# Optimization experiments

Hardware: AMD Instinct MI355X
Metric: run time of the kernel (lower is better)

## Reference

```python
import jax, jax.numpy as jnp
import numpy as np

B, TQ, TK, H = 8, 64, 8192, 256


def setup_inputs() -> dict:
    key = jax.random.key(0)
    k1, k2, k3, k4 = jax.random.split(key, 4)
    query = jax.random.normal(k1, (B, TQ, H), dtype=jnp.float32)
    keys = jax.random.normal(k2, (B, TK, H), dtype=jnp.float32)
    # nn.Linear(H, H): weight [H, H], bias [H]; scale like torch default-ish
    Wa_w = jax.random.normal(k3, (H, H), dtype=jnp.float32) * (1.0 / np.sqrt(H))
    Wa_b = jax.random.normal(k4, (H,), dtype=jnp.float32) * 0.01
    return {"query": query, "keys": keys, "Wa_w": Wa_w, "Wa_b": Wa_b}


def reference(query, keys, Wa_w, Wa_b):
    # keys_transformed = keys @ Wa_w.T + Wa_b  (torch Linear semantics)
    keys_t = jnp.einsum('bkh,oh->bko', keys, Wa_w) + Wa_b  # [B,TK,H]
    scores = jnp.einsum('bqh,bkh->bqk', query, keys_t)       # [B,TQ,TK]
    weights = jax.nn.softmax(scores, axis=-1)
    context = jnp.einsum('bqk,bkh->bqh', weights, keys)      # [B,TQ,H]
    return (context, weights)
```

## Files before the change

kernel.cpp:

```cpp
#include <hip/hip_runtime.h>

#define B 8
#define TQ 64
#define TK 8192
#define H 256

#define SPADB 72

#define KSPLIT 32
#define KPB (TK / KSPLIT)
#define CRS 72

typedef __attribute__((ext_vector_type(8))) short bf16x8;
typedef __attribute__((ext_vector_type(4))) float f32x4;
typedef __attribute__((ext_vector_type(4))) unsigned short u16x4;
typedef __attribute__((ext_vector_type(2))) unsigned int u32x2;

static __device__ inline unsigned short f2bf_rne(float x) {
    unsigned int u = __float_as_uint(x);
    unsigned int r = (u + 0x7fffu + ((u >> 16) & 1u)) >> 16;
    return (unsigned short)r;
}

__global__ __launch_bounds__(256) void qtransform_kernel(
    const float* __restrict__ query, const float* __restrict__ Wa_w,
    const float* __restrict__ Wa_b, unsigned short* __restrict__ qthi,
    unsigned short* __restrict__ qtlo, float* __restrict__ qb)
{
    __shared__ float q_s[H];
    __shared__ float red[4];
    const int r = blockIdx.x;
    const int t = threadIdx.x;
    q_s[t] = query[r * H + t];
    __syncthreads();

    float a0 = 0.f, a1 = 0.f, a2 = 0.f, a3 = 0.f;
    for (int o = 0; o < H; o += 4) {
        a0 += q_s[o + 0] * Wa_w[(o + 0) * H + t];
        a1 += q_s[o + 1] * Wa_w[(o + 1) * H + t];
        a2 += q_s[o + 2] * Wa_w[(o + 2) * H + t];
        a3 += q_s[o + 3] * Wa_w[(o + 3) * H + t];
    }
    const float s = (a0 + a1) + (a2 + a3);
    const unsigned int u = __float_as_uint(s);
    const float hif = __uint_as_float(u & 0xFFFF0000u);
    const float lof = s - hif;
    qthi[r * H + t] = (unsigned short)(u >> 16);
    qtlo[r * H + t] = (unsigned short)(__float_as_uint(lof) >> 16);

    float p = q_s[t] * Wa_b[t];
    for (int off = 32; off > 0; off >>= 1) p += __shfl_down(p, off, 64);
    if ((t & 63) == 0) red[t >> 6] = p;
    __syncthreads();
    if (t == 0) qb[r] = (red[0] + red[1]) + (red[2] + red[3]);
}

__global__ __launch_bounds__(256) void scores_kernel(
    const unsigned short* __restrict__ qthi, const unsigned short* __restrict__ qtlo,
    const float* __restrict__ qb, const float* __restrict__ keys,
    unsigned short* __restrict__ khi_ws, float* __restrict__ wout)
{
    __shared__ unsigned short a_hi[TQ][SPADB], a_lo[TQ][SPADB];
    __shared__ unsigned short b_hi[64][SPADB], b_lo[64][SPADB];
    const int t    = threadIdx.x;
    const int kt   = blockIdx.x;
    const int b    = blockIdx.y;
    const int k0g  = kt * 64;
    const int w    = t >> 6;
    const int lane = t & 63;
    const int lrow = lane & 15;
    const int lgrp = lane >> 4;

    f32x4 acc[4];
    #pragma unroll
    for (int nt = 0; nt < 4; ++nt) acc[nt] = (f32x4){0.f, 0.f, 0.f, 0.f};

    for (int hc = 0; hc < H; hc += 64) {
        __syncthreads();
        #pragma unroll
        for (int i = 0; i < 4; ++i) {
            int idx = t + 256 * i;
            int row = idx >> 4, hf = idx & 15;
            *(u16x4*)&a_hi[row][hf * 4] =
                *(const u16x4*)&qthi[(b * TQ + row) * H + hc + hf * 4];
            *(u16x4*)&a_lo[row][hf * 4] =
                *(const u16x4*)&qtlo[(b * TQ + row) * H + hc + hf * 4];
        }
        #pragma unroll
        for (int i = 0; i < 4; ++i) {
            int idx = t + 256 * i;
            int row = idx >> 4, hf = idx & 15;
            float4 vb = *(const float4*)&keys[(size_t)(b * TK + k0g + row) * H + hc + hf * 4];
            unsigned int u0 = __float_as_uint(vb.x), u1 = __float_as_uint(vb.y);
            unsigned int u2 = __float_as_uint(vb.z), u3 = __float_as_uint(vb.w);
            unsigned int h01 = (u0 >> 16) | (u1 & 0xFFFF0000u);
            unsigned int h23 = (u2 >> 16) | (u3 & 0xFFFF0000u);
            float l0 = vb.x - __uint_as_float(u0 & 0xFFFF0000u);
            float l1 = vb.y - __uint_as_float(u1 & 0xFFFF0000u);
            float l2 = vb.z - __uint_as_float(u2 & 0xFFFF0000u);
            float l3 = vb.w - __uint_as_float(u3 & 0xFFFF0000u);
            unsigned int l01 = (__float_as_uint(l0) >> 16) | (__float_as_uint(l1) & 0xFFFF0000u);
            unsigned int l23 = (__float_as_uint(l2) >> 16) | (__float_as_uint(l3) & 0xFFFF0000u);
            *(u32x2*)&b_hi[row][hf * 4] = (u32x2){h01, h23};
            *(u32x2*)&b_lo[row][hf * 4] = (u32x2){l01, l23};
            *(u32x2*)&khi_ws[((size_t)b * TK + k0g + row) * H + hc + hf * 4] = (u32x2){h01, h23};
        }
        __syncthreads();
        #pragma unroll
        for (int hs = 0; hs < 64; hs += 32) {
            bf16x8 ah = *(const bf16x8*)&a_hi[16 * w + lrow][hs + lgrp * 8];
            bf16x8 al = *(const bf16x8*)&a_lo[16 * w + lrow][hs + lgrp * 8];
            #pragma unroll
            for (int nt = 0; nt < 4; ++nt) {
                bf16x8 bh = *(const bf16x8*)&b_hi[16 * nt + lrow][hs + lgrp * 8];
                bf16x8 bl = *(const bf16x8*)&b_lo[16 * nt + lrow][hs + lgrp * 8];
                acc[nt] = __builtin_amdgcn_mfma_f32_16x16x32_bf16(ah, bh, acc[nt], 0, 0, 0);
                acc[nt] = __builtin_amdgcn_mfma_f32_16x16x32_bf16(ah, bl, acc[nt], 0, 0, 0);
                acc[nt] = __builtin_amdgcn_mfma_f32_16x16x32_bf16(al, bh, acc[nt], 0, 0, 0);
            }
        }
    }
    #pragma unroll
    for (int j = 0; j < 4; ++j) {
        const int qrow = 16 * w + lgrp * 4 + j;
        const float bias = qb[b * TQ + qrow];
        float* dst = &wout[(size_t)(b * TQ + qrow) * TK + k0g + lrow];
        #pragma unroll
        for (int nt = 0; nt < 4; ++nt) dst[16 * nt] = acc[nt][j] + bias;
    }
}

__global__ __launch_bounds__(1024) void softmax_kernel(
    float* __restrict__ w, unsigned short* __restrict__ phi)
{
    const int r = blockIdx.x;
    const int t = threadIdx.x;
    float4* row4 = (float4*)(w + (size_t)r * TK);
    __shared__ float redm[16];
    __shared__ float reds[16];
    const int wid = t >> 6, lane = t & 63;

    float4 v0 = row4[t];
    float4 v1 = row4[t + 1024];
    float m = fmaxf(fmaxf(fmaxf(v0.x, v0.y), fmaxf(v0.z, v0.w)),
                    fmaxf(fmaxf(v1.x, v1.y), fmaxf(v1.z, v1.w)));
    for (int off = 32; off > 0; off >>= 1) m = fmaxf(m, __shfl_xor(m, off, 64));
    if (lane == 0) redm[wid] = m;
    __syncthreads();
    m = redm[0];
    #pragma unroll
    for (int i = 1; i < 16; ++i) m = fmaxf(m, redm[i]);

    v0.x = __expf(v0.x - m); v0.y = __expf(v0.y - m);
    v0.z = __expf(v0.z - m); v0.w = __expf(v0.w - m);
    v1.x = __expf(v1.x - m); v1.y = __expf(v1.y - m);
    v1.z = __expf(v1.z - m); v1.w = __expf(v1.w - m);
    float s = (v0.x + v0.y + v0.z + v0.w) + (v1.x + v1.y + v1.z + v1.w);
    for (int off = 32; off > 0; off >>= 1) s += __shfl_xor(s, off, 64);
    if (lane == 0) reds[wid] = s;
    __syncthreads();
    s = reds[0];
    #pragma unroll
    for (int i = 1; i < 16; ++i) s += reds[i];
    const float inv = 1.0f / s;

    v0.x *= inv; v0.y *= inv; v0.z *= inv; v0.w *= inv;
    v1.x *= inv; v1.y *= inv; v1.z *= inv; v1.w *= inv;
    row4[t] = v0;
    row4[t + 1024] = v1;

    unsigned short* prow = phi + (size_t)r * TK;
    u16x4 p0, p1;
    p0[0] = f2bf_rne(v0.x); p0[1] = f2bf_rne(v0.y);
    p0[2] = f2bf_rne(v0.z); p0[3] = f2bf_rne(v0.w);
    p1[0] = f2bf_rne(v1.x); p1[1] = f2bf_rne(v1.y);
    p1[2] = f2bf_rne(v1.z); p1[3] = f2bf_rne(v1.w);
    *(u16x4*)&prow[t * 4] = p0;
    *(u16x4*)&prow[4096 + t * 4] = p1;
}

__global__ __launch_bounds__(256) void context_main_kernel(
    const unsigned short* __restrict__ phi, const unsigned short* __restrict__ khi,
    float* __restrict__ part)
{
    __shared__ unsigned short kT[64 * CRS];
    const int t    = threadIdx.x;
    const int ks   = blockIdx.x;
    const int ht   = blockIdx.y;
    const int b    = blockIdx.z;
    const int w    = t >> 6;
    const int lane = t & 63;
    const int lrow = lane & 15;
    const int lgrp = lane >> 4;

    f32x4 acc[4];
    #pragma unroll
    for (int nt = 0; nt < 4; ++nt) acc[nt] = (f32x4){0.f, 0.f, 0.f, 0.f};

    const int kbase = ks * KPB;
    for (int c = 0; c < KPB; c += 64) {
        __syncthreads();
        #pragma unroll
        for (int i = 0; i < 4; ++i) {
            int idx = t + 256 * i;
            int k = idx >> 4, hq = idx & 15;
            u16x4 v = *(const u16x4*)&khi[((size_t)b * TK + kbase + c + k) * H + ht * 64 + hq * 4];
            #pragma unroll
            for (int c4 = 0; c4 < 4; ++c4) {
                int h = hq * 4 + c4;
                kT[h * CRS + (((k >> 3) ^ ((h >> 3) & 7)) << 3) + (k & 7)] = v[c4];
            }
        }
        __syncthreads();
        #pragma unroll
        for (int kc = 0; kc < 64; kc += 32) {
            bf16x8 af = *(const bf16x8*)&phi[((size_t)(b * TQ) + 16 * w + lrow) * TK
                                             + kbase + c + kc + lgrp * 8];
            #pragma unroll
            for (int nt = 0; nt < 4; ++nt) {
                int h = 16 * nt + lrow;
                bf16x8 bf = *(const bf16x8*)&kT[h * CRS
                              + ((((kc >> 3) + lgrp) ^ ((h >> 3) & 7)) << 3)];
                acc[nt] = __builtin_amdgcn_mfma_f32_16x16x32_bf16(af, bf, acc[nt], 0, 0, 0);
            }
        }
    }
    float* dst = part + (size_t)ks * (B * TQ * H);
    #pragma unroll
    for (int j = 0; j < 4; ++j) {
        const int qrow = 16 * w + lgrp * 4 + j;
        #pragma unroll
        for (int nt = 0; nt < 4; ++nt)
            dst[(size_t)(b * TQ + qrow) * H + ht * 64 + 16 * nt + lrow] = acc[nt][j];
    }
}

__global__ __launch_bounds__(256) void context_reduce_kernel(
    const float* __restrict__ part, float* __restrict__ ctx)
{
    const int idx = blockIdx.x * 256 + threadIdx.x;
    float4 s = make_float4(0.f, 0.f, 0.f, 0.f);
    #pragma unroll 8
    for (int ks = 0; ks < KSPLIT; ++ks) {
        float4 v = *(const float4*)&part[(size_t)ks * (B * TQ * H) + (size_t)idx * 4];
        s.x += v.x; s.y += v.y; s.z += v.z; s.w += v.w;
    }
    *(float4*)&ctx[(size_t)idx * 4] = s;
}

extern "C" void kernel_launch(void* const* d_in, const int* in_sizes, int n_in,
                              void* d_out, int out_size, void* d_ws, size_t ws_size,
                              hipStream_t stream) {
    const float* query = (const float*)d_in[0];
    const float* keys  = (const float*)d_in[1];
    const float* Wa_w  = (const float*)d_in[2];
    const float* Wa_b  = (const float*)d_in[3];

    float* ctx = (float*)d_out;
    float* wts = (float*)d_out + B * TQ * H;

    char* p = (char*)d_ws;
    float* part = (float*)p;            p += (size_t)KSPLIT * B * TQ * H * 4;
    unsigned short* khi = (unsigned short*)p;  p += (size_t)B * TK * H * 2;
    unsigned short* phi = (unsigned short*)p;  p += (size_t)B * TQ * TK * 2;
    unsigned short* qthi = (unsigned short*)p; p += (size_t)B * TQ * H * 2;
    unsigned short* qtlo = (unsigned short*)p; p += (size_t)B * TQ * H * 2;
    float* qb = (float*)p;

    qtransform_kernel<<<B * TQ, 256, 0, stream>>>(query, Wa_w, Wa_b, qthi, qtlo, qb);
    scores_kernel<<<dim3(TK / 64, B), 256, 0, stream>>>(qthi, qtlo, qb, keys, khi, wts);
    softmax_kernel<<<B * TQ, 1024, 0, stream>>>(wts, phi);
    context_main_kernel<<<dim3(KSPLIT, 4, B), 256, 0, stream>>>(phi, khi, part);
    context_reduce_kernel<<<(B * TQ * H / 4) / 256, 256, 0, stream>>>(part, ctx);
}
```

Before: 158.9 us.

## Store bf16 keys transposed, double-buffer scores staging, drop LDS in context GEMM

The scores kernel now writes the bf16 keys copy transposed ([B,H,TK]) so the context GEMM can load B-fragments directly from global memory, with no LDS transpose and no barriers. The scores kernel reads query fragments straight from global instead of staging them through LDS. It also double-buffers the key tiles with register prefetch of the next chunk, and uses an XOR-swizzled unpadded LDS layout. The transposed key writes are 2-byte scattered stores with stride TK, which may be poorly coalesced and could slow the scores kernel.

Result: slower. 187.5 us (+18.0%).

```diff
diff --git a/kernel.cpp b/kernel.cpp
--- a/kernel.cpp
+++ b/kernel.cpp
@@ -5,11 +5,8 @@
 #define TK 8192
 #define H 256
 
-#define SPADB 72
-
 #define KSPLIT 32
 #define KPB (TK / KSPLIT)
-#define CRS 72
 
 typedef __attribute__((ext_vector_type(8))) short bf16x8;
 typedef __attribute__((ext_vector_type(4))) float f32x4;
@@ -55,13 +52,59 @@
     if (t == 0) qb[r] = (red[0] + red[1]) + (red[2] + red[3]);
 }
 
-__global__ __launch_bounds__(256) void scores_kernel(
+
+#define STAGE1(v, row, buf, khb) {                                             \
+    unsigned int u0=__float_as_uint(v.x), u1=__float_as_uint(v.y);             \
+    unsigned int u2=__float_as_uint(v.z), u3=__float_as_uint(v.w);             \
+    unsigned int h01=(u0>>16)|(u1&0xFFFF0000u), h23=(u2>>16)|(u3&0xFFFF0000u); \
+    float l0=v.x-__uint_as_float(u0&0xFFFF0000u);                              \
+    float l1=v.y-__uint_as_float(u1&0xFFFF0000u);                              \
+    float l2=v.z-__uint_as_float(u2&0xFFFF0000u);                              \
+    float l3=v.w-__uint_as_float(u3&0xFFFF0000u);                              \
+    unsigned int q01=(__float_as_uint(l0)>>16)|(__float_as_uint(l1)&0xFFFF0000u); \
+    unsigned int q23=(__float_as_uint(l2)>>16)|(__float_as_uint(l3)&0xFFFF0000u); \
+    int bo=(row)*128 + (((hf>>1)^((row)&7))<<4) + ((hf&1)<<3);                 \
+    *(u32x2*)((char*)b_hi[buf]+bo) = (u32x2){h01,h23};                         \
+    *(u32x2*)((char*)b_lo[buf]+bo) = (u32x2){q01,q23};                         \
+    khb[(size_t)(hf*4+0)*TK + (row)] = (unsigned short)(u0>>16);               \
+    khb[(size_t)(hf*4+1)*TK + (row)] = (unsigned short)(u1>>16);               \
+    khb[(size_t)(hf*4+2)*TK + (row)] = (unsigned short)(u2>>16);               \
+    khb[(size_t)(hf*4+3)*TK + (row)] = (unsigned short)(u3>>16); }
+
+#define LOADCHUNK(d0,d1,d2,d3, hc)                                             \
+    d0 = *(const float4*)&kbase_g[(size_t)(sr +  0) * H + (hc) + hf * 4];      \
+    d1 = *(const float4*)&kbase_g[(size_t)(sr + 16) * H + (hc) + hf * 4];      \
+    d2 = *(const float4*)&kbase_g[(size_t)(sr + 32) * H + (hc) + hf * 4];      \
+    d3 = *(const float4*)&kbase_g[(size_t)(sr + 48) * H + (hc) + hf * 4];
+
+#define STAGECHUNK(v0,v1,v2,v3, buf, hc) {                                     \
+    unsigned short* khb = khiT + ((size_t)b * H + (hc)) * TK + k0g;            \
+    STAGE1(v0, sr +  0, buf, khb); STAGE1(v1, sr + 16, buf, khb);              \
+    STAGE1(v2, sr + 32, buf, khb); STAGE1(v3, sr + 48, buf, khb); }
+
+#define COMPUTE(buf, hc) {                                                     \
+    _Pragma("unroll")                                                          \
+    for (int hs = 0; hs < 64; hs += 32) {                                      \
+        bf16x8 ah = *(const bf16x8*)&ah_base[(hc) + hs + lgrp * 8];            \
+        bf16x8 al = *(const bf16x8*)&al_base[(hc) + hs + lgrp * 8];            \
+        _Pragma("unroll")                                                      \
+        for (int nt = 0; nt < 4; ++nt) {                                       \
+            int rr = 16 * nt + lrow;                                           \
+            int rb = rr * 128 + ((((hs >> 3) + lgrp) ^ (rr & 7)) << 4);        \
+            bf16x8 bh = *(const bf16x8*)((const char*)b_hi[buf] + rb);         \
+            bf16x8 bl = *(const bf16x8*)((const char*)b_lo[buf] + rb);         \
+            acc[nt] = __builtin_amdgcn_mfma_f32_16x16x32_bf16(ah, bh, acc[nt], 0, 0, 0); \
+            acc[nt] = __builtin_amdgcn_mfma_f32_16x16x32_bf16(ah, bl, acc[nt], 0, 0, 0); \
+            acc[nt] = __builtin_amdgcn_mfma_f32_16x16x32_bf16(al, bh, acc[nt], 0, 0, 0); \
+        } } }
+
+__global__ __launch_bounds__(256, 4) void scores_kernel(
     const unsigned short* __restrict__ qthi, const unsigned short* __restrict__ qtlo,
     const float* __restrict__ qb, const float* __restrict__ keys,
-    unsigned short* __restrict__ khi_ws, float* __restrict__ wout)
-{
-    __shared__ unsigned short a_hi[TQ][SPADB], a_lo[TQ][SPADB];
-    __shared__ unsigned short b_hi[64][SPADB], b_lo[64][SPADB];
+    unsigned short* __restrict__ khiT, float* __restrict__ wout)
+{
+    __shared__ unsigned short b_hi[2][64 * 64];
+    __shared__ unsigned short b_lo[2][64 * 64];
     const int t    = threadIdx.x;
     const int kt   = blockIdx.x;
     const int b    = blockIdx.y;
@@ -70,56 +113,39 @@
     const int lane = t & 63;
     const int lrow = lane & 15;
     const int lgrp = lane >> 4;
+    const int sr   = t >> 4;
+    const int hf   = t & 15;
+
+    const float* kbase_g = keys + (size_t)(b * TK + k0g) * H;
+    const unsigned short* ah_base = qthi + (size_t)(b * TQ + 16 * w + lrow) * H;
+    const unsigned short* al_base = qtlo + (size_t)(b * TQ + 16 * w + lrow) * H;
 
     f32x4 acc[4];
     #pragma unroll
     for (int nt = 0; nt < 4; ++nt) acc[nt] = (f32x4){0.f, 0.f, 0.f, 0.f};
 
-    for (int hc = 0; hc < H; hc += 64) {
-        __syncthreads();
-        #pragma unroll
-        for (int i = 0; i < 4; ++i) {
-            int idx = t + 256 * i;
-            int row = idx >> 4, hf = idx & 15;
-            *(u16x4*)&a_hi[row][hf * 4] =
-                *(const u16x4*)&qthi[(b * TQ + row) * H + hc + hf * 4];
-            *(u16x4*)&a_lo[row][hf * 4] =
-                *(const u16x4*)&qtlo[(b * TQ + row) * H + hc + hf * 4];
-        }
-        #pragma unroll
-        for (int i = 0; i < 4; ++i) {
-            int idx = t + 256 * i;
-            int row = idx >> 4, hf = idx & 15;
-            float4 vb = *(const float4*)&keys[(size_t)(b * TK + k0g + row) * H + hc + hf * 4];
-            unsigned int u0 = __float_as_uint(vb.x), u1 = __float_as_uint(vb.y);
-            unsigned int u2 = __float_as_uint(vb.z), u3 = __float_as_uint(vb.w);
-            unsigned int h01 = (u0 >> 16) | (u1 & 0xFFFF0000u);
-            unsigned int h23 = (u2 >> 16) | (u3 & 0xFFFF0000u);
-            float l0 = vb.x - __uint_as_float(u0 & 0xFFFF0000u);
-            float l1 = vb.y - __uint_as_float(u1 & 0xFFFF0000u);
-            float l2 = vb.z - __uint_as_float(u2 & 0xFFFF0000u);
-            float l3 = vb.w - __uint_as_float(u3 & 0xFFFF0000u);
-            unsigned int l01 = (__float_as_uint(l0) >> 16) | (__float_as_uint(l1) & 0xFFFF0000u);
-            unsigned int l23 = (__float_as_uint(l2) >> 16) | (__float_as_uint(l3) & 0xFFFF0000u);
-            *(u32x2*)&b_hi[row][hf * 4] = (u32x2){h01, h23};
-            *(u32x2*)&b_lo[row][hf * 4] = (u32x2){l01, l23};
-            *(u32x2*)&khi_ws[((size_t)b * TK + k0g + row) * H + hc + hf * 4] = (u32x2){h01, h23};
-        }
-        __syncthreads();
-        #pragma unroll
-        for (int hs = 0; hs < 64; hs += 32) {
-            bf16x8 ah = *(const bf16x8*)&a_hi[16 * w + lrow][hs + lgrp * 8];
-            bf16x8 al = *(const bf16x8*)&a_lo[16 * w + lrow][hs + lgrp * 8];
-            #pragma unroll
-            for (int nt = 0; nt < 4; ++nt) {
-                bf16x8 bh = *(const bf16x8*)&b_hi[16 * nt + lrow][hs + lgrp * 8];
-                bf16x8 bl = *(const bf16x8*)&b_lo[16 * nt + lrow][hs + lgrp * 8];
-                acc[nt] = __builtin_amdgcn_mfma_f32_16x16x32_bf16(ah, bh, acc[nt], 0, 0, 0);
-                acc[nt] = __builtin_amdgcn_mfma_f32_16x16x32_bf16(ah, bl, acc[nt], 0, 0, 0);
-                acc[nt] = __builtin_amdgcn_mfma_f32_16x16x32_bf16(al, bh, acc[nt], 0, 0, 0);
-            }
-        }
-    }
+    float4 a0, a1, a2, a3, c0, c1, c2, c3;
+    LOADCHUNK(a0, a1, a2, a3, 0)
+
+    LOADCHUNK(c0, c1, c2, c3, 64)
+    STAGECHUNK(a0, a1, a2, a3, 0, 0)
+    __syncthreads();
+    COMPUTE(0, 0)
+
+    LOADCHUNK(a0, a1, a2, a3, 128)
+    STAGECHUNK(c0, c1, c2, c3, 1, 64)
+    __syncthreads();
+    COMPUTE(1, 64)
+
+    LOADCHUNK(c0, c1, c2, c3, 192)
+    STAGECHUNK(a0, a1, a2, a3, 0, 128)
+    __syncthreads();
+    COMPUTE(0, 128)
+
+    STAGECHUNK(c0, c1, c2, c3, 1, 192)
+    __syncthreads();
+    COMPUTE(1, 192)
+
     #pragma unroll
     for (int j = 0; j < 4; ++j) {
         const int qrow = 16 * w + lgrp * 4 + j;
@@ -180,10 +206,9 @@
 }
 
 __global__ __launch_bounds__(256) void context_main_kernel(
-    const unsigned short* __restrict__ phi, const unsigned short* __restrict__ khi,
+    const unsigned short* __restrict__ phi, const unsigned short* __restrict__ khiT,
     float* __restrict__ part)
 {
-    __shared__ unsigned short kT[64 * CRS];
     const int t    = threadIdx.x;
     const int ks   = blockIdx.x;
     const int ht   = blockIdx.y;
@@ -192,37 +217,24 @@
     const int lane = t & 63;
     const int lrow = lane & 15;
     const int lgrp = lane >> 4;
+    const int kbase = ks * KPB;
+
+    const unsigned short* arow = phi + (size_t)(b * TQ + 16 * w + lrow) * TK
+                                     + kbase + lgrp * 8;
+    const unsigned short* brow = khiT + (size_t)(b * H + ht * 64 + lrow) * TK
+                                      + kbase + lgrp * 8;
 
     f32x4 acc[4];
     #pragma unroll
     for (int nt = 0; nt < 4; ++nt) acc[nt] = (f32x4){0.f, 0.f, 0.f, 0.f};
 
-    const int kbase = ks * KPB;
-    for (int c = 0; c < KPB; c += 64) {
-        __syncthreads();
+    #pragma unroll 2
+    for (int c = 0; c < KPB; c += 32) {
+        bf16x8 af = *(const bf16x8*)&arow[c];
         #pragma unroll
-        for (int i = 0; i < 4; ++i) {
-            int idx = t + 256 * i;
-            int k = idx >> 4, hq = idx & 15;
-            u16x4 v = *(const u16x4*)&khi[((size_t)b * TK + kbase + c + k) * H + ht * 64 + hq * 4];
-            #pragma unroll
-            for (int c4 = 0; c4 < 4; ++c4) {
-                int h = hq * 4 + c4;
-                kT[h * CRS + (((k >> 3) ^ ((h >> 3) & 7)) << 3) + (k & 7)] = v[c4];
-            }
-        }
-        __syncthreads();
-        #pragma unroll
-        for (int kc = 0; kc < 64; kc += 32) {
-            bf16x8 af = *(const bf16x8*)&phi[((size_t)(b * TQ) + 16 * w + lrow) * TK
-                                             + kbase + c + kc + lgrp * 8];
-            #pragma unroll
-            for (int nt = 0; nt < 4; ++nt) {
-                int h = 16 * nt + lrow;
-                bf16x8 bf = *(const bf16x8*)&kT[h * CRS
-                              + ((((kc >> 3) + lgrp) ^ ((h >> 3) & 7)) << 3)];
-                acc[nt] = __builtin_amdgcn_mfma_f32_16x16x32_bf16(af, bf, acc[nt], 0, 0, 0);
-            }
+        for (int nt = 0; nt < 4; ++nt) {
+            bf16x8 bfg = *(const bf16x8*)&brow[(size_t)(16 * nt) * TK + c];
+            acc[nt] = __builtin_amdgcn_mfma_f32_16x16x32_bf16(af, bfg, acc[nt], 0, 0, 0);
         }
     }
     float* dst = part + (size_t)ks * (B * TQ * H);
@@ -260,16 +272,16 @@
     float* wts = (float*)d_out + B * TQ * H;
 
     char* p = (char*)d_ws;
-    float* part = (float*)p;            p += (size_t)KSPLIT * B * TQ * H * 4;
-    unsigned short* khi = (unsigned short*)p;  p += (size_t)B * TK * H * 2;
-    unsigned short* phi = (unsigned short*)p;  p += (size_t)B * TQ * TK * 2;
-    unsigned short* qthi = (unsigned short*)p; p += (size_t)B * TQ * H * 2;
-    unsigned short* qtlo = (unsigned short*)p; p += (size_t)B * TQ * H * 2;
+    float* part = (float*)p;                    p += (size_t)KSPLIT * B * TQ * H * 4;
+    unsigned short* khiT = (unsigned short*)p;  p += (size_t)B * H * TK * 2;
+    unsigned short* phi = (unsigned short*)p;   p += (size_t)B * TQ * TK * 2;
+    unsigned short* qthi = (unsigned short*)p;  p += (size_t)B * TQ * H * 2;
+    unsigned short* qtlo = (unsigned short*)p;  p += (size_t)B * TQ * H * 2;
     float* qb = (float*)p;
 
     qtransform_kernel<<<B * TQ, 256, 0, stream>>>(query, Wa_w, Wa_b, qthi, qtlo, qb);
-    scores_kernel<<<dim3(TK / 64, B), 256, 0, stream>>>(qthi, qtlo, qb, keys, khi, wts);
+    scores_kernel<<<dim3(TK / 64, B), 256, 0, stream>>>(qthi, qtlo, qb, keys, khiT, wts);
     softmax_kernel<<<B * TQ, 1024, 0, stream>>>(wts, phi);
-    context_main_kernel<<<dim3(KSPLIT, 4, B), 256, 0, stream>>>(phi, khi, part);
+    context_main_kernel<<<dim3(KSPLIT, 4, B), 256, 0, stream>>>(phi, khiT, part);
     context_reduce_kernel<<<(B * TQ * H / 4) / 256, 256, 0, stream>>>(part, ctx);
 }
```
